# Kernel tuning notes

Hardware: AMD Instinct MI355X
Metric: run time of the kernel (lower is better)

The kernel has to match this reference:

```python
import jax, jax.numpy as jnp
import numpy as np
import math

# Model constants (from module source)
E = 384      # n_embd
H = 6        # n_head
D = E // H   # head_size = 64
L = 6        # n_layer
T_BLK = 36   # block_size
S = 210      # num_of_stations
B = 1024     # batch
PM25_MIN = 0.0
PM25_MAX = 500.0
LN_EPS = 1e-5


def sinusoidal_position_embedding(seq_len, dim):
    pos = jnp.arange(seq_len, dtype=jnp.float32)[:, None]
    div = jnp.exp(jnp.arange(0, dim, 2, dtype=jnp.float32) * (-math.log(10000.0) / dim))
    pe = jnp.zeros((seq_len, dim), dtype=jnp.float32)
    pe = pe.at[:, 0::2].set(jnp.sin(pos * div))
    pe = pe.at[:, 1::2].set(jnp.cos(pos * div))
    return pe


def layernorm(x, g, b):
    m = jnp.mean(x, axis=-1, keepdims=True)
    v = jnp.var(x, axis=-1, keepdims=True)
    return (x - m) / jnp.sqrt(v + LN_EPS) * g + b


def setup_inputs() -> dict:
    key = jax.random.key(0)
    ks = iter(jax.random.split(key, 32))
    sd = 0.02
    inp = {
        "idx": jax.random.randint(next(ks), (B, T_BLK, S, 2), 0, 10, dtype=jnp.int64 if jax.config.read('jax_enable_x64') else jnp.int32),
        "targets": jax.random.randint(next(ks), (B, T_BLK, 2), 0, 10),
        "ix": 0,
        "stn_ix": 5,
        # embeddings / input projection
        "Wp": jax.random.normal(next(ks), (S, E), jnp.float32) * sd,
        "bp": jnp.zeros((E,), jnp.float32),
        "station_emb": jax.random.normal(next(ks), (S, E), jnp.float32) * sd,
        "fire_emb": jax.random.normal(next(ks), (10, E), jnp.float32) * sd,
        # per-layer transformer params (leading dim = L)
        "ln1_g": jnp.ones((L, E), jnp.float32),
        "ln1_b": jnp.zeros((L, E), jnp.float32),
        "Wq": jax.random.normal(next(ks), (L, E, E), jnp.float32) * sd,
        "Wk": jax.random.normal(next(ks), (L, E, E), jnp.float32) * sd,
        "Wv": jax.random.normal(next(ks), (L, E, E), jnp.float32) * sd,
        "Wo": jax.random.normal(next(ks), (L, E, E), jnp.float32) * sd,
        "bo": jnp.zeros((L, E), jnp.float32),
        "ln2_g": jnp.ones((L, E), jnp.float32),
        "ln2_b": jnp.zeros((L, E), jnp.float32),
        "W1": jax.random.normal(next(ks), (L, E, 4 * E), jnp.float32) * sd,
        "b1": jnp.zeros((L, 4 * E), jnp.float32),
        "W2": jax.random.normal(next(ks), (L, 4 * E, E), jnp.float32) * sd,
        "b2": jnp.zeros((L, E), jnp.float32),
        # final norm + head
        "lnf_g": jnp.ones((E,), jnp.float32),
        "lnf_b": jnp.zeros((E,), jnp.float32),
        "Wh": jax.random.normal(next(ks), (E, 1), jnp.float32) * sd,
        "bh": jnp.zeros((1,), jnp.float32),
    }
    return inp


def reference(idx, targets, ix, stn_ix, Wp, bp, station_emb, fire_emb,
              ln1_g, ln1_b, Wq, Wk, Wv, Wo, bo, ln2_g, ln2_b,
              W1, b1, W2, b2, lnf_g, lnf_b, Wh, bh):
    # eval mode: dropout layers are identity
    Bsz, T, Snum, _ = idx.shape
    pm25 = idx[..., 0].astype(jnp.float32)            # [B,T,S]
    fire = idx[:, :, stn_ix, 1]                        # [B,T] int
    norm_pm25 = (pm25 - PM25_MIN) / (PM25_MAX - PM25_MIN)
    x = (norm_pm25 @ Wp + bp                           # pm25 projection [B,T,E]
         + fire_emb[fire]                              # fire embedding  [B,T,E]
         + station_emb[stn_ix]                         # spatial emb broadcast
         + sinusoidal_position_embedding(T, E))        # positional emb

    causal = jnp.tril(jnp.ones((T, T), dtype=bool))
    scale = D ** (-0.5)
    for l in range(L):
        h = layernorm(x, ln1_g[l], ln1_b[l])
        q = (h @ Wq[l]).reshape(Bsz, T, H, D)
        k = (h @ Wk[l]).reshape(Bsz, T, H, D)
        v = (h @ Wv[l]).reshape(Bsz, T, H, D)
        w = jnp.einsum('bthd,bshd->bhts', q, k) * scale
        w = jnp.where(causal, w, -jnp.inf)
        w = jax.nn.softmax(w, axis=-1)
        o = jnp.einsum('bhts,bshd->bthd', w, v).reshape(Bsz, T, E)
        x = x + (o @ Wo[l] + bo[l])
        h2 = layernorm(x, ln2_g[l], ln2_b[l])
        x = x + (jax.nn.relu(h2 @ W1[l] + b1[l]) @ W2[l] + b2[l])

    x = layernorm(x, lnf_g, lnf_b)
    logits = jax.nn.sigmoid(x @ Wh + bh)               # [B,T,1]

    tgt = targets[..., 0:1].astype(jnp.float32)        # [B,T,1]
    norm_tgt = (tgt - PM25_MIN) / (PM25_MAX - PM25_MIN)
    mse_loss = jnp.mean((logits - norm_tgt) ** 2)
    denorm = logits * (PM25_MAX - PM25_MIN) + PM25_MIN
    y = tgt.reshape(-1)
    yhat = denorm.reshape(-1)
    r2 = 1.0 - jnp.sum((y - yhat) ** 2) / jnp.sum((y - jnp.mean(y)) ** 2)
    return (denorm, mse_loss, r2)
```

## Files before the change

kernel.cpp:

```cpp
#include <hip/hip_runtime.h>
#include <hip/hip_fp8.h>
#include <stdint.h>


#define EDIM   384
#define NHEAD  6
#define DHEAD  64
#define NLAYER 6
#define TBLK   36
#define SNUM   210
#define BSZ    1024
#define NTOK   (BSZ*TBLK)
#define QKVSTR 1152
#define KPM    256
#define NHBLK  (NTOK/4)

typedef __attribute__((ext_vector_type(4))) float floatx4;
typedef __attribute__((ext_vector_type(4))) unsigned int uintx4;

static __device__ __forceinline__ unsigned char f2fp8(float f){
  __hip_fp8_e4m3 t(f); return t.__x;
}
static __device__ __forceinline__ float fp82f(unsigned char u){
  __hip_fp8_e4m3 t; t.__x = u; return (float)t;
}
static __device__ __forceinline__ void gld_lds16(const void* g, void* l){
  __builtin_amdgcn_global_load_lds(
      (const __attribute__((address_space(1))) void*)g,
      (__attribute__((address_space(3))) void*)l, 16, 0, 0);
}

__global__ __launch_bounds__(256) void wt_transpose(const float* __restrict__ in,
    unsigned char* __restrict__ out, int K, int M, long outStride){
  __shared__ float tile[32][33];
  const int mat = blockIdx.z;
  const float* src = in + (size_t)mat*K*M;
  unsigned char* dst = out + (size_t)mat*outStride;
  const int m0 = blockIdx.x*32, k0 = blockIdx.y*32;
  const int tx = threadIdx.x, ty = threadIdx.y;
  for(int i=ty;i<32;i+=8) tile[i][tx] = src[(size_t)(k0+i)*M + m0+tx];
  __syncthreads();
  for(int i=ty;i<32;i+=8) dst[(size_t)(m0+i)*K + k0+tx] = f2fp8(tile[tx][i]);
}

__global__ __launch_bounds__(256) void wp_transpose(const float* __restrict__ Wp,
    unsigned char* __restrict__ wp_t){
  const int m = blockIdx.x, k = threadIdx.x;
  wp_t[(size_t)m*KPM + k] = (k < SNUM) ? f2fp8(Wp[(size_t)k*EDIM + m]) : 0;
}

__global__ __launch_bounds__(256) void prep_pm(const int* __restrict__ idx,
    unsigned char* __restrict__ pm){
  const long i = (long)blockIdx.x*256 + threadIdx.x;
  if(i >= (long)NTOK*KPM) return;
  const int row = i / KPM, s = i - (long)row*KPM;
  float v = 0.f;
  if(s < SNUM) v = (float)idx[((size_t)row*SNUM + s)*2] * (256.f/500.f);
  pm[i] = f2fp8(v);
}

__global__ __launch_bounds__(256) void prep_fire(const int* __restrict__ idx,
    const int* __restrict__ stn_p, int* __restrict__ fire){
  const int row = blockIdx.x*256 + threadIdx.x;
  if(row < NTOK) fire[row] = idx[((size_t)row*SNUM + stn_p[0])*2 + 1];
}

__global__ __launch_bounds__(384) void pe_kernel(float* __restrict__ pe){
  const int t = blockIdx.x, e = threadIdx.x;
  const float freq = __expf(-(float)(2*(e>>1)) * (9.210340371976184f/384.f));
  const float ang = (float)t * freq;
  pe[t*EDIM + e] = (e & 1) ? __cosf(ang) : __sinf(ang);
}

__global__ __launch_bounds__(256) void ln_act(const float* __restrict__ x,
    const float* __restrict__ g, const float* __restrict__ b,
    unsigned char* __restrict__ out){
  const int wave = threadIdx.x >> 6, lane = threadIdx.x & 63;
  const int row = blockIdx.x*4 + wave;
  const float* xr = x + (size_t)row*EDIM;
  float v[6]; float s=0.f, sq=0.f;
  #pragma unroll
  for(int j=0;j<6;j++){ v[j]=xr[j*64+lane]; s+=v[j]; sq+=v[j]*v[j]; }
  #pragma unroll
  for(int m=1;m<64;m<<=1){ s += __shfl_xor(s,m); sq += __shfl_xor(sq,m); }
  const float mean = s*(1.f/384.f);
  const float var  = sq*(1.f/384.f) - mean*mean;
  const float rstd = rsqrtf(var + 1e-5f);
  unsigned char* orow = out + (size_t)row*EDIM;
  #pragma unroll
  for(int j=0;j<6;j++){
    int e = j*64+lane;
    orow[e] = f2fp8((v[j]-mean)*rstd*g[e] + b[e]);
  }
}

template<int MODE, bool RELU>
__global__ __launch_bounds__(256) void gemm_k(const unsigned char* __restrict__ A,
    const unsigned char* __restrict__ Wt, const float* __restrict__ bias,
    unsigned char* __restrict__ outb, float* __restrict__ xout,
    const int* __restrict__ fire, const float* __restrict__ pe,
    const float* __restrict__ stat_emb, const int* __restrict__ stn_p,
    const float* __restrict__ fire_emb, int M, int K){
  __shared__ __align__(16) unsigned char As[2][128*64];
  __shared__ __align__(16) unsigned char Bs[2][128*64];
  const int tid  = threadIdx.x;
  const int m0   = blockIdx.x * 128;
  const int n0   = blockIdx.y * 128;
  const int wave = tid >> 6, lane = tid & 63;
  const int wr = wave >> 1, wc = wave & 1;
  const int lrow = lane & 15, quad = lane >> 4;
  const int lsw = (lrow & 3) ^ ((lrow >> 2) & 3);
  floatx4 acc[4][4];
  #pragma unroll
  for(int i=0;i<4;i++)
    #pragma unroll
    for(int j=0;j<4;j++) acc[i][j] = (floatx4){0.f,0.f,0.f,0.f};

  const int S = K >> 6;
  auto stage = [&](int s, int bi){
    const int kk = s*64;
    #pragma unroll
    for(int p=0;p<2;p++){
      int i = tid + p*256;
      int r = i >> 2, jp = i & 3;
      int jl = jp ^ (r & 3) ^ ((r >> 2) & 3);
      gld_lds16(&A [(size_t)(n0+r)*K + kk + jl*16], &As[bi][i*16]);
      gld_lds16(&Wt[(size_t)(m0+r)*K + kk + jl*16], &Bs[bi][i*16]);
    }
  };
  stage(0, 0);
  for(int s=0; s<S; s++){
    const int bi = s & 1;
    __syncthreads();
    if(s+1 < S) stage(s+1, bi^1);
    #pragma unroll
    for(int ks=0; ks<2; ks++){
      const int joff = (((ks*2 + (quad>>1)) ^ lsw) << 4) + (quad & 1)*8;
      long af[4], bfv[4];
      #pragma unroll
      for(int ti=0;ti<4;ti++)
        af[ti]  = *(const long*)(&As[bi][(wr*64+ti*16+lrow)*64 + joff]);
      #pragma unroll
      for(int tj=0;tj<4;tj++)
        bfv[tj] = *(const long*)(&Bs[bi][(wc*64+tj*16+lrow)*64 + joff]);
      #pragma unroll
      for(int ti=0;ti<4;ti++)
        #pragma unroll
        for(int tj=0;tj<4;tj++)
          acc[ti][tj] = __builtin_amdgcn_mfma_f32_16x16x32_fp8_fp8(af[ti], bfv[tj], acc[ti][tj], 0,0,0);
    }
  }
  if(MODE==0){
    __syncthreads();
    unsigned char* Cs = (unsigned char*)&As[0][0];
    #pragma unroll
    for(int ti=0;ti<4;ti++){
      #pragma unroll
      for(int tj=0;tj<4;tj++){
        const int col = wc*64 + tj*16 + lrow;
        const float bi = bias ? bias[m0+col] : 0.f;
        #pragma unroll
        for(int r=0;r<4;r++){
          const int row = wr*64 + ti*16 + quad*4 + r;
          float val = acc[ti][tj][r] + bi;
          if(RELU) val = fmaxf(val, 0.f);
          Cs[row*128 + col] = f2fp8(val);
        }
      }
    }
    __syncthreads();
    #pragma unroll
    for(int p=0;p<4;p++){
      const int q = tid + p*256;
      const int row = q >> 3, c16 = (q & 7)*16;
      *(uintx4*)(&outb[(size_t)(n0+row)*M + m0 + c16]) =
          *(const uintx4*)(&Cs[row*128 + c16]);
    }
  } else {
    const int stn = (MODE==2) ? stn_p[0] : 0;
    #pragma unroll
    for(int ti=0;ti<4;ti++){
      #pragma unroll
      for(int r=0;r<4;r++){
        int row = n0 + wr*64 + ti*16 + quad*4 + r;
        int fidx = 0, trow = 0;
        if(MODE==2){ fidx = fire[row]; trow = row % TBLK; }
        #pragma unroll
        for(int tj=0;tj<4;tj++){
          int col = m0 + wc*64 + tj*16 + lrow;
          float val = acc[ti][tj][r];
          if(MODE==1){
            xout[(size_t)row*EDIM + col] += val + bias[col];
          } else {
            val = val*(1.f/256.f) + bias[col] + stat_emb[(size_t)stn*EDIM + col]
                + pe[trow*EDIM + col] + fire_emb[(size_t)fidx*EDIM + col];
            xout[(size_t)row*EDIM + col] = val;
          }
        }
      }
    }
  }
}

__global__ __launch_bounds__(512, 4) void gemm_row_ln(
    const unsigned char* __restrict__ A, const unsigned char* __restrict__ Wt,
    const float* __restrict__ bias, float* __restrict__ x,
    const float* __restrict__ g, const float* __restrict__ b,
    unsigned char* __restrict__ h, int K, int writeH){
  __shared__ __align__(16) unsigned char As[2][64*32];
  __shared__ __align__(16) unsigned char Bs[2][384*32];
  const int tid = threadIdx.x;
  const int n0 = blockIdx.x * 64;
  const int wave = tid >> 6, lane = tid & 63;
  const int rw = wave >> 1, cw = wave & 1;
  const int lrow = lane & 15, quad = lane >> 4;
  const int xsw = ((lane >> 2) & 1) << 4;
  floatx4 acc[12];
  #pragma unroll
  for(int j=0;j<12;j++) acc[j] = (floatx4){0.f,0.f,0.f,0.f};

  const int S = K >> 5;
  auto stage = [&](int s, int bi){
    const int kk = s*32;
    if(tid < 128){
      int r = tid >> 1, c = (((tid&1) ^ ((tid>>3)&1))) * 16;
      gld_lds16(&A[(size_t)(n0+r)*K + kk + c], &As[bi][tid*16]);
    }
    {
      int i = tid;
      int r = i >> 1, c = (((i&1) ^ ((i>>3)&1))) * 16;
      gld_lds16(&Wt[(size_t)r*K + kk + c], &Bs[bi][i*16]);
    }
    if(tid < 256){
      int i = tid + 512;
      int r = i >> 1, c = (((i&1) ^ ((i>>3)&1))) * 16;
      gld_lds16(&Wt[(size_t)r*K + kk + c], &Bs[bi][i*16]);
    }
  };
  stage(0, 0);
  for(int s=0; s<S; s++){
    const int bi = s & 1;
    __syncthreads();
    if(s+1 < S) stage(s+1, bi^1);
    long af = *(const long*)(&As[bi][(rw*16+lrow)*32 + ((quad*8) ^ xsw)]);
    long bfv[12];
    #pragma unroll
    for(int tj=0;tj<12;tj++)
      bfv[tj] = *(const long*)(&Bs[bi][(cw*192+tj*16+lrow)*32 + ((quad*8) ^ xsw)]);
    #pragma unroll
    for(int tj=0;tj<12;tj++)
      acc[tj] = __builtin_amdgcn_mfma_f32_16x16x32_fp8_fp8(af, bfv[tj], acc[tj], 0,0,0);
  }
  __syncthreads();
  float* part = (float*)&As[0][0];
  {
    float ps[4] = {0.f,0.f,0.f,0.f}, pq[4] = {0.f,0.f,0.f,0.f};
    #pragma unroll
    for(int tj=0;tj<12;tj++){
      const int col = cw*192 + tj*16 + lrow;
      const float bi = bias[col];
      #pragma unroll
      for(int r=0;r<4;r++){
        const int row = n0 + rw*16 + quad*4 + r;
        float v = acc[tj][r] + bi + x[(size_t)row*EDIM + col];
        acc[tj][r] = v;
        ps[r] += v; pq[r] += v*v;
      }
    }
    #pragma unroll
    for(int r=0;r<4;r++){
      #pragma unroll
      for(int m=1;m<16;m<<=1){ ps[r] += __shfl_xor(ps[r],m); pq[r] += __shfl_xor(pq[r],m); }
    }
    if(lrow == 0){
      #pragma unroll
      for(int r=0;r<4;r++){
        const int rl = rw*16 + quad*4 + r;
        part[rl*2 + cw]       = ps[r];
        part[128 + rl*2 + cw] = pq[r];
      }
    }
  }
  __syncthreads();
  #pragma unroll
  for(int r=0;r<4;r++){
    const int rl = rw*16 + quad*4 + r;
    const int row = n0 + rl;
    const float s = part[rl*2+0] + part[rl*2+1];
    const float q = part[128+rl*2+0] + part[128+rl*2+1];
    const float mean = s*(1.f/384.f);
    const float var  = q*(1.f/384.f) - mean*mean;
    const float rstd = rsqrtf(var + 1e-5f);
    #pragma unroll
    for(int tj=0;tj<12;tj++){
      const int col = cw*192 + tj*16 + lrow;
      const float v = acc[tj][r];
      x[(size_t)row*EDIM + col] = v;
      if(writeH)
        h[(size_t)row*EDIM + col] = f2fp8((v-mean)*rstd*g[col] + b[col]);
    }
  }
}

__global__ __launch_bounds__(256) void attn_kernel(const unsigned char* __restrict__ qkv,
    unsigned char* __restrict__ o){
  const int bh = blockIdx.x;
  const int b = bh / NHEAD, h = bh % NHEAD;
  const int wave = threadIdx.x >> 6, lane = threadIdx.x & 63;
  const int tid = threadIdx.x;
  __shared__ float qs[TBLK*64];
  __shared__ float ks[TBLK*65];
  __shared__ float ps[TBLK*64];
  const size_t base = (size_t)b*TBLK*QKVSTR + h*DHEAD;
  const unsigned char* qp = qkv + base;
  const unsigned char* kp = qkv + base + 384;
  const unsigned char* vp = qkv + base + 768;
  for(int i=tid; i<TBLK*16; i+=256){
    int t = i >> 4, d4 = (i & 15) * 4;
    unsigned int rq = *(const unsigned int*)&qp[(size_t)t*QKVSTR + d4];
    unsigned int rk = *(const unsigned int*)&kp[(size_t)t*QKVSTR + d4];
    #pragma unroll
    for(int j=0;j<4;j++){
      qs[t*64 + d4 + j] = fp82f((unsigned char)(rq >> (8*j)));
      ks[t*65 + d4 + j] = fp82f((unsigned char)(rk >> (8*j)));
    }
  }
  float vreg[TBLK];
  #pragma unroll
  for(int s2=0;s2<TBLK;s2++) vreg[s2] = fp82f(vp[(size_t)s2*QKVSTR + lane]);
  __syncthreads();
  const int krow = (lane < TBLK) ? lane : (TBLK-1);
  float kreg[64];
  #pragma unroll
  for(int dd=0;dd<64;dd++) kreg[dd] = ks[krow*65 + dd];
  const float scale = 0.125f;
  #pragma unroll
  for(int j=0;j<9;j++){
    const int t = wave + 4*j;
    float d = 0.f;
    #pragma unroll
    for(int gg=0;gg<16;gg++){
      float4 q4 = *(const float4*)&qs[t*64 + gg*4];
      d = fmaf(q4.x, kreg[gg*4+0], d);
      d = fmaf(q4.y, kreg[gg*4+1], d);
      d = fmaf(q4.z, kreg[gg*4+2], d);
      d = fmaf(q4.w, kreg[gg*4+3], d);
    }
    float val = (lane <= t) ? d*scale : -INFINITY;
    float mx = val;
    #pragma unroll
    for(int m=1;m<64;m<<=1) mx = fmaxf(mx, __shfl_xor(mx,m));
    float p = __expf(val - mx);
    float sum = p;
    #pragma unroll
    for(int m=1;m<64;m<<=1) sum += __shfl_xor(sum,m);
    ps[t*64 + lane] = p / sum;
  }
  __syncthreads();
  #pragma unroll
  for(int j=0;j<9;j++){
    const int t = wave + 4*j;
    float acc = 0.f;
    #pragma unroll
    for(int gg=0;gg<9;gg++){
      float4 p4 = *(const float4*)&ps[t*64 + gg*4];
      acc = fmaf(p4.x, vreg[gg*4+0], acc);
      acc = fmaf(p4.y, vreg[gg*4+1], acc);
      acc = fmaf(p4.z, vreg[gg*4+2], acc);
      acc = fmaf(p4.w, vreg[gg*4+3], acc);
    }
    o[(size_t)b*TBLK*EDIM + (size_t)t*EDIM + h*DHEAD + lane] = f2fp8(acc);
  }
}

__global__ __launch_bounds__(256) void head_kernel(const float* __restrict__ x,
    const float* __restrict__ g, const float* __restrict__ b,
    const float* __restrict__ Wh, const float* __restrict__ bh,
    const int* __restrict__ targets, float* __restrict__ out,
    float* __restrict__ partials){
  const int wave = threadIdx.x >> 6, lane = threadIdx.x & 63;
  const int row = blockIdx.x*4 + wave;
  const float* xr = x + (size_t)row*EDIM;
  float v[6]; float s=0.f, sq=0.f;
  #pragma unroll
  for(int j=0;j<6;j++){ v[j]=xr[j*64+lane]; s+=v[j]; sq+=v[j]*v[j]; }
  #pragma unroll
  for(int m=1;m<64;m<<=1){ s += __shfl_xor(s,m); sq += __shfl_xor(sq,m); }
  const float mean = s*(1.f/384.f);
  const float var  = sq*(1.f/384.f) - mean*mean;
  const float rstd = rsqrtf(var + 1e-5f);
  float dot = 0.f;
  #pragma unroll
  for(int j=0;j<6;j++){
    int e = j*64+lane;
    float hh = (v[j]-mean)*rstd*g[e] + b[e];
    dot = fmaf(hh, Wh[e], dot);
  }
  #pragma unroll
  for(int m=1;m<64;m<<=1) dot += __shfl_xor(dot,m);
  __shared__ float part[4][4];
  if(lane == 0){
    float logit = 1.f/(1.f + __expf(-(dot + bh[0])));
    float den = logit * 500.f;
    out[row] = den;
    float tgt = (float)targets[(size_t)row*2];
    float nt  = tgt * (1.f/500.f);
    part[wave][0] = (logit-nt)*(logit-nt);
    part[wave][1] = (tgt-den)*(tgt-den);
    part[wave][2] = tgt;
    part[wave][3] = tgt*tgt;
  }
  __syncthreads();
  if(threadIdx.x < 4){
    float t0 = part[0][threadIdx.x] + part[1][threadIdx.x]
             + part[2][threadIdx.x] + part[3][threadIdx.x];
    partials[(size_t)threadIdx.x*NHBLK + blockIdx.x] = t0;
  }
}

__global__ __launch_bounds__(1024) void finalize_reduce(
    const float* __restrict__ partials, float* __restrict__ out){
  __shared__ float red[16];
  const int tid = threadIdx.x;
  const int c = tid >> 8, j = tid & 255;
  float s = 0.f;
  for(int i = j; i < NHBLK; i += 256) s += partials[(size_t)c*NHBLK + i];
  #pragma unroll
  for(int m=1;m<64;m<<=1) s += __shfl_xor(s,m);
  if((tid & 63) == 0) red[tid >> 6] = s;
  __syncthreads();
  if(tid == 0){
    float a0 = red[0]+red[1]+red[2]+red[3];
    float a1 = red[4]+red[5]+red[6]+red[7];
    float a2 = red[8]+red[9]+red[10]+red[11];
    float a3 = red[12]+red[13]+red[14]+red[15];
    const float n = (float)NTOK;
    out[NTOK]   = a0 / n;
    float denom = a3 - a2*a2/n;
    out[NTOK+1] = 1.f - a1/denom;
  }
}

extern "C" void kernel_launch(void* const* d_in, const int* in_sizes, int n_in,
                              void* d_out, int out_size, void* d_ws, size_t ws_size,
                              hipStream_t stream){
  (void)in_sizes; (void)n_in; (void)out_size; (void)ws_size;
  const int*   idx      = (const int*)  d_in[0];
  const int*   targets  = (const int*)  d_in[1];
  const int*   stn_ix   = (const int*)  d_in[3];
  const float* Wp       = (const float*)d_in[4];
  const float* bp       = (const float*)d_in[5];
  const float* stat_emb = (const float*)d_in[6];
  const float* fire_emb = (const float*)d_in[7];
  const float* ln1_g    = (const float*)d_in[8];
  const float* ln1_b    = (const float*)d_in[9];
  const float* Wq       = (const float*)d_in[10];
  const float* Wk       = (const float*)d_in[11];
  const float* Wv       = (const float*)d_in[12];
  const float* Wo       = (const float*)d_in[13];
  const float* bo       = (const float*)d_in[14];
  const float* ln2_g    = (const float*)d_in[15];
  const float* ln2_b    = (const float*)d_in[16];
  const float* W1       = (const float*)d_in[17];
  const float* b1       = (const float*)d_in[18];
  const float* W2       = (const float*)d_in[19];
  const float* b2       = (const float*)d_in[20];
  const float* lnf_g    = (const float*)d_in[21];
  const float* lnf_b    = (const float*)d_in[22];
  const float* Wh       = (const float*)d_in[23];
  const float* bh       = (const float*)d_in[24];
  float* out = (float*)d_out;

  char* ws = (char*)d_ws;
  float*         x      = (float*)        (ws + 0);
  unsigned char* h      = (unsigned char*)(ws + 56623104);
  unsigned char* qkv    = (unsigned char*)(ws + 84934656);
  unsigned char* obuf   = (unsigned char*)(ws + 169869312);
  unsigned char* ffn    = qkv;
  unsigned char* pm     = (unsigned char*)(ws + 169869312);
  int*           fire   = (int*)          (ws + 186384384);
  unsigned char* wp_t   = (unsigned char*)(ws + 186531840);
  float*         pe     = (float*)        (ws + 186703872);
  float*         partials = (float*)      (ws + 169869312);
  unsigned char* wqkv_t = (unsigned char*)(ws + 198180864);
  unsigned char* wo_t   = (unsigned char*)(ws + 203489280);
  unsigned char* w1_t   = (unsigned char*)(ws + 205258752);
  unsigned char* w2_t   = (unsigned char*)(ws + 212336640);

  const dim3 tb(32,8);
  wt_transpose<<<dim3(12,12,6), tb, 0, stream>>>(Wq, wqkv_t,          384,  384, 442368);
  wt_transpose<<<dim3(12,12,6), tb, 0, stream>>>(Wk, wqkv_t + 147456, 384,  384, 442368);
  wt_transpose<<<dim3(12,12,6), tb, 0, stream>>>(Wv, wqkv_t + 294912, 384,  384, 442368);
  wt_transpose<<<dim3(12,12,6), tb, 0, stream>>>(Wo, wo_t,            384,  384, 147456);
  wt_transpose<<<dim3(48,12,6), tb, 0, stream>>>(W1, w1_t,            384, 1536, 589824);
  wt_transpose<<<dim3(12,48,6), tb, 0, stream>>>(W2, w2_t,           1536,  384, 589824);
  wp_transpose<<<384, 256, 0, stream>>>(Wp, wp_t);
  pe_kernel<<<TBLK, 384, 0, stream>>>(pe);
  prep_pm<<<(NTOK*KPM + 255)/256, 256, 0, stream>>>(idx, pm);
  prep_fire<<<(NTOK + 255)/256, 256, 0, stream>>>(idx, stn_ix, fire);

  gemm_k<2,false><<<dim3(3,288), 256, 0, stream>>>(pm, wp_t, bp, nullptr, x,
      fire, pe, stat_emb, stn_ix, fire_emb, 384, KPM);

  ln_act<<<NTOK/4, 256, 0, stream>>>(x, ln1_g, ln1_b, h);

  const dim3 gQKV(9, 288);
  const dim3 gE(3, 288);
  const dim3 gF(12, 288);
  for(int l=0; l<NLAYER; l++){
    gemm_k<0,false><<<gQKV, 256, 0, stream>>>(h, wqkv_t + (size_t)l*442368,
        nullptr, qkv, nullptr, nullptr, nullptr, nullptr, nullptr, nullptr, 1152, 384);
    attn_kernel<<<BSZ*NHEAD, 256, 0, stream>>>(qkv, obuf);
    gemm_row_ln<<<NTOK/64, 512, 0, stream>>>(obuf, wo_t + (size_t)l*147456,
        bo + l*EDIM, x, ln2_g + l*EDIM, ln2_b + l*EDIM, h, 384, 1);
    gemm_k<0,true><<<gF, 256, 0, stream>>>(h, w1_t + (size_t)l*589824,
        b1 + l*1536, ffn, nullptr, nullptr, nullptr, nullptr, nullptr, nullptr, 1536, 384);
    gemm_k<1,false><<<gE, 256, 0, stream>>>(ffn, w2_t + (size_t)l*589824,
        b2 + l*EDIM, nullptr, x, nullptr, nullptr, nullptr, nullptr, nullptr, 384, 1536);
    if(l < NLAYER-1)
      ln_act<<<NTOK/4, 256, 0, stream>>>(x, ln1_g + (l+1)*EDIM, ln1_b + (l+1)*EDIM, h);
  }

  head_kernel<<<NHBLK, 256, 0, stream>>>(x, lnf_g, lnf_b, Wh, bh, targets, out, partials);
  finalize_reduce<<<1, 1024, 0, stream>>>(partials, out);
}
```

Measured before the change: 2.078 ms.

## Rewrite attention kernel with MFMA, one wave per batch-head

The attention kernel now gives each wavefront its own (batch, head) pair, so each block covers four heads. QK^T is computed with fp8 16x16x32 MFMA directly from the fp8 qkv buffer. P·V is computed with bf16 MFMA, with P and a transposed, zero-padded V staged in LDS. The output goes through LDS and is written with 16-byte stores. This replaces scalar FMA loops and block-wide syncs, at the cost of padding the 36-token sequence to 48/64 and reading Q/K rows past the sequence end. For the last batch those reads go beyond the qkv buffer.

```diff
diff --git a/kernel.cpp b/kernel.cpp
--- a/kernel.cpp
+++ b/kernel.cpp
@@ -17,12 +17,18 @@
 
 typedef __attribute__((ext_vector_type(4))) float floatx4;
 typedef __attribute__((ext_vector_type(4))) unsigned int uintx4;
+typedef __attribute__((ext_vector_type(8))) short short8;
 
 static __device__ __forceinline__ unsigned char f2fp8(float f){
   __hip_fp8_e4m3 t(f); return t.__x;
 }
 static __device__ __forceinline__ float fp82f(unsigned char u){
   __hip_fp8_e4m3 t; t.__x = u; return (float)t;
+}
+static __device__ __forceinline__ unsigned short f2bf(float f){
+  union { float fv; unsigned int u; } v; v.fv = f;
+  unsigned int r = v.u + 0x7FFFu + ((v.u >> 16) & 1u);
+  return (unsigned short)(r >> 16);
 }
 static __device__ __forceinline__ void gld_lds16(const void* g, void* l){
   __builtin_amdgcn_global_load_lds(
@@ -304,72 +310,109 @@
 
 __global__ __launch_bounds__(256) void attn_kernel(const unsigned char* __restrict__ qkv,
     unsigned char* __restrict__ o){
-  const int bh = blockIdx.x;
+  __shared__ __align__(16) unsigned short lds[4*8064];
+  const int wave = threadIdx.x >> 6, lane = threadIdx.x & 63;
+  const int bh = blockIdx.x*4 + wave;
   const int b = bh / NHEAD, h = bh % NHEAD;
-  const int wave = threadIdx.x >> 6, lane = threadIdx.x & 63;
-  const int tid = threadIdx.x;
-  __shared__ float qs[TBLK*64];
-  __shared__ float ks[TBLK*65];
-  __shared__ float ps[TBLK*64];
+  const int lrow = lane & 15, quad = lane >> 4;
+  unsigned short* PT = lds + wave*8064;
+  unsigned short* VT = PT + 48*72;
   const size_t base = (size_t)b*TBLK*QKVSTR + h*DHEAD;
   const unsigned char* qp = qkv + base;
   const unsigned char* kp = qkv + base + 384;
   const unsigned char* vp = qkv + base + 768;
-  for(int i=tid; i<TBLK*16; i+=256){
-    int t = i >> 4, d4 = (i & 15) * 4;
-    unsigned int rq = *(const unsigned int*)&qp[(size_t)t*QKVSTR + d4];
-    unsigned int rk = *(const unsigned int*)&kp[(size_t)t*QKVSTR + d4];
-    #pragma unroll
-    for(int j=0;j<4;j++){
-      qs[t*64 + d4 + j] = fp82f((unsigned char)(rq >> (8*j)));
-      ks[t*65 + d4 + j] = fp82f((unsigned char)(rk >> (8*j)));
-    }
-  }
-  float vreg[TBLK];
-  #pragma unroll
-  for(int s2=0;s2<TBLK;s2++) vreg[s2] = fp82f(vp[(size_t)s2*QKVSTR + lane]);
-  __syncthreads();
-  const int krow = (lane < TBLK) ? lane : (TBLK-1);
-  float kreg[64];
-  #pragma unroll
-  for(int dd=0;dd<64;dd++) kreg[dd] = ks[krow*65 + dd];
+
+  for(int s=0;s<64;s++){
+    float v = (s < TBLK) ? fp82f(vp[(size_t)s*QKVSTR + lane]) : 0.f;
+    VT[lane*72 + s] = f2bf(v);
+  }
+  #pragma unroll
+  for(int i=lane;i<96;i+=64){
+    int row = i >> 1, c = (i & 1)*8;
+    *(short8*)(&PT[row*72 + 48 + c]) = (short8){0,0,0,0,0,0,0,0};
+  }
+
+  floatx4 accs[3][3];
+  #pragma unroll
+  for(int i=0;i<3;i++)
+    #pragma unroll
+    for(int j=0;j<3;j++) accs[i][j] = (floatx4){0.f,0.f,0.f,0.f};
+  #pragma unroll
+  for(int ks=0;ks<2;ks++){
+    long aq[3], bk[3];
+    #pragma unroll
+    for(int ti=0;ti<3;ti++)
+      aq[ti] = *(const long*)(qp + (size_t)(ti*16+lrow)*QKVSTR + ks*32 + quad*8);
+    #pragma unroll
+    for(int tj=0;tj<3;tj++)
+      bk[tj] = *(const long*)(kp + (size_t)(tj*16+lrow)*QKVSTR + ks*32 + quad*8);
+    #pragma unroll
+    for(int ti=0;ti<3;ti++)
+      #pragma unroll
+      for(int tj=0;tj<3;tj++)
+        accs[ti][tj] = __builtin_amdgcn_mfma_f32_16x16x32_fp8_fp8(aq[ti], bk[tj], accs[ti][tj], 0,0,0);
+  }
+
   const float scale = 0.125f;
   #pragma unroll
-  for(int j=0;j<9;j++){
-    const int t = wave + 4*j;
-    float d = 0.f;
-    #pragma unroll
-    for(int gg=0;gg<16;gg++){
-      float4 q4 = *(const float4*)&qs[t*64 + gg*4];
-      d = fmaf(q4.x, kreg[gg*4+0], d);
-      d = fmaf(q4.y, kreg[gg*4+1], d);
-      d = fmaf(q4.z, kreg[gg*4+2], d);
-      d = fmaf(q4.w, kreg[gg*4+3], d);
-    }
-    float val = (lane <= t) ? d*scale : -INFINITY;
-    float mx = val;
-    #pragma unroll
-    for(int m=1;m<64;m<<=1) mx = fmaxf(mx, __shfl_xor(mx,m));
-    float p = __expf(val - mx);
-    float sum = p;
-    #pragma unroll
-    for(int m=1;m<64;m<<=1) sum += __shfl_xor(sum,m);
-    ps[t*64 + lane] = p / sum;
-  }
-  __syncthreads();
-  #pragma unroll
-  for(int j=0;j<9;j++){
-    const int t = wave + 4*j;
-    float acc = 0.f;
-    #pragma unroll
-    for(int gg=0;gg<9;gg++){
-      float4 p4 = *(const float4*)&ps[t*64 + gg*4];
-      acc = fmaf(p4.x, vreg[gg*4+0], acc);
-      acc = fmaf(p4.y, vreg[gg*4+1], acc);
-      acc = fmaf(p4.z, vreg[gg*4+2], acc);
-      acc = fmaf(p4.w, vreg[gg*4+3], acc);
-    }
-    o[(size_t)b*TBLK*EDIM + (size_t)t*EDIM + h*DHEAD + lane] = f2fp8(acc);
+  for(int ti=0;ti<3;ti++){
+    #pragma unroll
+    for(int r=0;r<4;r++){
+      const int t = ti*16 + quad*4 + r;
+      float pv[3]; float mx = -INFINITY;
+      #pragma unroll
+      for(int tj=0;tj<3;tj++){
+        const int s = tj*16 + lrow;
+        pv[tj] = (s <= t) ? accs[ti][tj][r]*scale : -INFINITY;
+        mx = fmaxf(mx, pv[tj]);
+      }
+      #pragma unroll
+      for(int m=1;m<16;m<<=1) mx = fmaxf(mx, __shfl_xor(mx, m));
+      float sum = 0.f;
+      #pragma unroll
+      for(int tj=0;tj<3;tj++){ pv[tj] = __expf(pv[tj]-mx); sum += pv[tj]; }
+      #pragma unroll
+      for(int m=1;m<16;m<<=1) sum += __shfl_xor(sum, m);
+      const float rs = 1.f/sum;
+      #pragma unroll
+      for(int tj=0;tj<3;tj++)
+        PT[t*72 + tj*16 + lrow] = f2bf(pv[tj]*rs);
+    }
+  }
+
+  floatx4 acco[3][4];
+  #pragma unroll
+  for(int i=0;i<3;i++)
+    #pragma unroll
+    for(int j=0;j<4;j++) acco[i][j] = (floatx4){0.f,0.f,0.f,0.f};
+  #pragma unroll
+  for(int ks=0;ks<2;ks++){
+    short8 ap[3], bv[4];
+    #pragma unroll
+    for(int ti=0;ti<3;ti++)
+      ap[ti] = *(const short8*)(&PT[(ti*16+lrow)*72 + ks*32 + quad*8]);
+    #pragma unroll
+    for(int td=0;td<4;td++)
+      bv[td] = *(const short8*)(&VT[(td*16+lrow)*72 + ks*32 + quad*8]);
+    #pragma unroll
+    for(int ti=0;ti<3;ti++)
+      #pragma unroll
+      for(int td=0;td<4;td++)
+        acco[ti][td] = __builtin_amdgcn_mfma_f32_16x16x32_bf16(ap[ti], bv[td], acco[ti][td], 0,0,0);
+  }
+
+  unsigned char* OB = (unsigned char*)VT;
+  #pragma unroll
+  for(int ti=0;ti<3;ti++)
+    #pragma unroll
+    for(int td=0;td<4;td++)
+      #pragma unroll
+      for(int r=0;r<4;r++)
+        OB[(ti*16+quad*4+r)*80 + td*16 + lrow] = f2fp8(acco[ti][td][r]);
+  for(int i=lane;i<TBLK*4;i+=64){
+    const int row = i >> 2, c16 = (i & 3)*16;
+    *(uintx4*)(&o[((size_t)b*TBLK+row)*EDIM + h*DHEAD + c16]) =
+        *(const uintx4*)(&OB[row*80 + c16]);
   }
 }
 
@@ -510,7 +553,7 @@
   for(int l=0; l<NLAYER; l++){
     gemm_k<0,false><<<gQKV, 256, 0, stream>>>(h, wqkv_t + (size_t)l*442368,
         nullptr, qkv, nullptr, nullptr, nullptr, nullptr, nullptr, nullptr, 1152, 384);
-    attn_kernel<<<BSZ*NHEAD, 256, 0, stream>>>(qkv, obuf);
+    attn_kernel<<<BSZ*NHEAD/4, 256, 0, stream>>>(qkv, obuf);
     gemm_row_ln<<<NTOK/64, 512, 0, stream>>>(obuf, wo_t + (size_t)l*147456,
         bo + l*EDIM, x, ln2_g + l*EDIM, ln2_b + l*EDIM, h, 384, 1);
     gemm_k<0,true><<<gF, 256, 0, stream>>>(h, w1_t + (size_t)l*589824,
```

Measured after the change: 1.890 ms. -9.0%, faster.
